# Kernel optimization log

Hardware: AMD Instinct MI355X
Metric: run time of the kernel (lower is better)

The kernel has to match this reference:

```python
import jax, jax.numpy as jnp
import numpy as np

RES = 64
NU = 0.002
DX = 2.0 * np.pi / RES
DT = 0.001
M1 = 12
M2 = 12
WIDTH = 32


def _central(x, axis, dx):
    # periodic central difference via roll (matches torch.roll semantics)
    return (jnp.roll(x, -1, axis) - jnp.roll(x, 1, axis)) / (2.0 * dx)


def _grad_module(u):
    # TurbulenceRCLN.compute_grad_u: central diff in x,y; j==2 branch is u*0.1 (kept faithfully)
    g0 = _central(u, 2, DX)
    g1 = _central(u, 3, DX)
    g2 = u * 0.1
    return jnp.stack([g0, g1, g2], axis=2)  # (B,3,3,N,N,N) indexed [b,i,j]


def _grad_solver(u):
    # NavierStokesSolver._compute_gradient: true central differences in all 3 dirs
    return jnp.stack([_central(u, 2 + j, DX) for j in range(3)], axis=2)


def _laplacian(u):
    lap = jnp.zeros_like(u)
    for ax in (2, 3, 4):
        lap = lap + (jnp.roll(u, -1, ax) - 2.0 * u + jnp.roll(u, 1, ax)) / (DX * DX)
    return lap


def _div_tau(tau):
    # tau: (B,3,3,N,N,N); div_i = sum_j d tau_ij / dx_j
    return sum(_central(tau[:, :, j], 2 + j, DX) for j in range(3))


def _spectral_conv(x, w1, w2):
    # x: (B,C,N,N); w1/w2: (C,C,M1,M2,2) real/imag
    N = x.shape[-1]
    xft = jnp.fft.rfft2(x)  # (B,C,N,N//2+1) complex
    w1c = w1[..., 0] + 1j * w1[..., 1]
    w2c = w2[..., 0] + 1j * w2[..., 1]
    a = jnp.einsum('bixy,ioxy->boxy', xft[:, :, :M1, :M2], w1c)
    b = jnp.einsum('bixy,ioxy->boxy', xft[:, :, -M1:, :M2], w2c)
    out = jnp.zeros_like(xft).at[:, :, :M1, :M2].set(a).at[:, :, -M1:, :M2].set(b)
    return jnp.fft.irfft2(out, s=(N, N))


def _fno2d(x, fc0_w, fc0_b, spec_w1, spec_w2, conv_w, conv_b, fc1_w, fc1_b, fc2_w, fc2_b):
    h = jnp.einsum('bcxy,cd->bdxy', x, fc0_w) + fc0_b[None, :, None, None]
    for l in range(4):
        s = _spectral_conv(h, spec_w1[l], spec_w2[l])
        w = jnp.einsum('bcxy,co->boxy', h, conv_w[l]) + conv_b[l][None, :, None, None]
        h = s + w
        if l < 3:
            h = jax.nn.gelu(h)
    h = jax.nn.gelu(jnp.einsum('bcxy,cd->bdxy', h, fc1_w) + fc1_b[None, :, None, None])
    return jnp.einsum('bcxy,cd->bdxy', h, fc2_w) + fc2_b[None, :, None, None]


def setup_inputs() -> dict:
    key = jax.random.key(0)
    ks = jax.random.split(key, 8)
    B = 16
    scale = 1.0 / (WIDTH * WIDTH)
    return {
        'velocity': jax.random.normal(ks[0], (B, 3, RES, RES, RES), jnp.float32),
        'fc0_w': jax.random.normal(ks[1], (10, WIDTH), jnp.float32) * 0.1,
        'fc0_b': jnp.zeros((WIDTH,), jnp.float32),
        'spec_w1': jax.random.normal(ks[2], (4, WIDTH, WIDTH, M1, M2, 2), jnp.float32) * scale,
        'spec_w2': jax.random.normal(ks[3], (4, WIDTH, WIDTH, M1, M2, 2), jnp.float32) * scale,
        'conv_w': jax.random.normal(ks[4], (4, WIDTH, WIDTH), jnp.float32) * 0.1,
        'conv_b': jnp.zeros((4, WIDTH), jnp.float32),
        'fc1_w': jax.random.normal(ks[5], (WIDTH, 128), jnp.float32) * 0.1,
        'fc1_b': jnp.zeros((128,), jnp.float32),
        'fc2_w': jax.random.normal(ks[6], (128, 6), jnp.float32) * 0.1,
        'fc2_b': jnp.zeros((6,), jnp.float32),
    }


def reference(velocity, fc0_w, fc0_b, spec_w1, spec_w2, conv_w, conv_b, fc1_w, fc1_b, fc2_w, fc2_b):
    B = velocity.shape[0]
    N = RES
    # --- soft-shell closure input ---
    grad_u = _grad_module(velocity)                                   # (B,3,3,N,N,N)
    S = 0.5 * (grad_u + jnp.swapaxes(grad_u, 1, 2))
    S_mag = jnp.sqrt(2.0 * jnp.sum(S * S, axis=(1, 2), keepdims=True))  # (B,1,1,N,N,N)
    g_slice = grad_u[:, :, :, :, N // 2, :].reshape(B, 9, N, N)        # 9 grad channels at mid-plane
    s_slice = S_mag[:, :, :, :, N // 2, :].reshape(B, 1, N, N)         # 1 strain-mag channel
    closure_in = jnp.concatenate([g_slice, s_slice], axis=1)          # (B,10,N,N)
    tau2d = _fno2d(closure_in, fc0_w, fc0_b, spec_w1, spec_w2, conv_w, conv_b,
                   fc1_w, fc1_b, fc2_w, fc2_b)                         # (B,6,N,N)
    t = jnp.broadcast_to(tau2d[..., None], (B, 6, N, N, N))           # expand along z
    # reconstruct symmetric stress tensor (B,3,3,N,N,N)
    row0 = jnp.stack([t[:, 0], t[:, 3], t[:, 4]], axis=1)
    row1 = jnp.stack([t[:, 3], t[:, 1], t[:, 5]], axis=1)
    row2 = jnp.stack([t[:, 4], t[:, 5], t[:, 2]], axis=1)
    tau_full = jnp.stack([row0, row1, row2], axis=1)
    # --- hard-core NS step ---
    g = _grad_solver(velocity)
    lap = _laplacian(velocity)
    convection = jnp.einsum('bixyz,bijxyz->bjxyz', velocity, g)
    div_tau = _div_tau(tau_full)
    return velocity + DT * (-convection + NU * lap + div_tau)
```

## Files before the change

kernel.cpp:

```cpp
#include <hip/hip_runtime.h>
#include <math.h>

#define NRES 64
#define NXY  4096
#define NVOL 262144
#define BB   16
#define WID  32
#define MM   12
#define R24  24

constexpr double DX_d   = 2.0 * 3.14159265358979323846 / 64.0;
constexpr float  INV2DX = (float)(1.0 / (2.0 * DX_d));
constexpr float  INVDX2 = (float)(1.0 / (DX_d * DX_d));
constexpr float  DT_c   = 0.001f;
constexpr float  NU_c   = 0.002f;

constexpr size_t OFF_FR  = 0;
constexpr size_t OFF_FI  = OFF_FR + (size_t)R24 * NRES;
constexpr size_t OFF_GR  = OFF_FI + (size_t)R24 * NRES;
constexpr size_t OFF_GI  = OFF_GR + (size_t)MM * NRES;
constexpr size_t OFF_CL  = OFF_GI + (size_t)MM * NRES;
constexpr size_t OFF_HA  = OFF_CL + (size_t)BB * 10 * NXY;
constexpr size_t OFF_HB  = OFF_HA + (size_t)BB * WID * NXY;
constexpr size_t OFF_T1R = OFF_HB + (size_t)BB * WID * NXY;
constexpr size_t OFF_T1I = OFF_T1R + (size_t)BB * WID * R24 * NRES;
constexpr size_t OFF_XR  = OFF_T1I + (size_t)BB * WID * R24 * NRES;
constexpr size_t OFF_XI  = OFF_XR + (size_t)BB * WID * R24 * MM;
constexpr size_t OFF_MR  = OFF_XI + (size_t)BB * WID * R24 * MM;
constexpr size_t OFF_MI  = OFF_MR + (size_t)BB * WID * R24 * MM;
constexpr size_t OFF_AR  = OFF_MI + (size_t)BB * WID * R24 * MM;
constexpr size_t OFF_AI  = OFF_AR + (size_t)BB * WID * MM * NRES;
constexpr size_t OFF_H1  = OFF_AI + (size_t)BB * WID * MM * NRES;
constexpr size_t OFF_TAU = OFF_H1 + (size_t)BB * 128 * NXY;
constexpr size_t OFF_FRT = OFF_TAU + (size_t)BB * 6 * NXY;
constexpr size_t OFF_FIT = OFF_FRT + (size_t)NRES * R24;

constexpr size_t OFF_SP  = OFF_H1;
constexpr size_t OFF_W1T = OFF_H1 + (size_t)BB * WID * NXY;
constexpr size_t OFF_CWT = OFF_W1T + 4096;
constexpr size_t OFF_W0T = OFF_CWT + 4096;
constexpr size_t OFF_PT  = OFF_T1R;
constexpr size_t PT_STRIDE = (size_t)BB * 6 * NXY;

__device__ __forceinline__ float gelu_fast(float x) {
    float z = 0.79788456080286535588f * (x + 0.044715f * x * x * x);
    float e = __expf(2.0f * z);
    float t = 1.0f - 2.0f / (e + 1.0f);
    return 0.5f * x * (1.0f + t);
}

__global__ void k_setup(const float* __restrict__ fc1w, const float* __restrict__ convw,
                        const float* __restrict__ fc0w, float* __restrict__ ws) {
    int idx = blockIdx.x * 256 + threadIdx.x;
    if (idx < R24 * NRES) {
        int r = idx / NRES, x = idx % NRES;
        int kx = (r < MM) ? r : (r + 40);
        double ang = -2.0 * 3.14159265358979323846 * (double)(kx * x) / 64.0;
        float cr = (float)cos(ang), ci = (float)sin(ang);
        ws[OFF_FR + idx] = cr;
        ws[OFF_FI + idx] = ci;
        ws[OFF_FRT + (size_t)x * R24 + r] = cr;
        ws[OFF_FIT + (size_t)x * R24 + r] = ci;
    }
    if (idx < MM * NRES) {
        int ky = idx / NRES, y = idx % NRES;
        double ang = -2.0 * 3.14159265358979323846 * (double)(ky * y) / 64.0;
        ws[OFF_GR + idx] = (float)cos(ang);
        ws[OFF_GI + idx] = (float)sin(ang);
    }
    if (idx < 4096) {
        int c = idx >> 7, e = idx & 127;
        ws[OFF_W1T + (size_t)e * 32 + c] = fc1w[idx];
    } else if (idx < 8192) {
        int j = idx - 4096;
        int l = j >> 10, r = j & 1023;
        int c = r >> 5, o = r & 31;
        ws[OFF_CWT + (size_t)l * 1024 + o * 32 + c] = convw[j];
    } else if (idx < 8512) {
        int j = idx - 8192;
        int c = j >> 5, d = j & 31;
        ws[OFF_W0T + (size_t)d * 10 + c] = fc0w[j];
    }
}

__global__ void k_closure(const float* __restrict__ v, float* __restrict__ ws) {
    int idx = blockIdx.x * 256 + threadIdx.x;
    int b = idx >> 10;
    int rr = idx & 1023;
    int x = rr >> 4, z0 = (rr & 15) * 4;
    int xp = (x + 1) & 63, xm = (x - 1) & 63;
    float4 g[3][3];
    for (int i = 0; i < 3; i++) {
        const float* vb = v + (((size_t)(b * 3 + i)) << 18);
        float4 u4   = *(const float4*)(vb + (size_t)x  * 4096 + 32 * 64 + z0);
        float4 uxp4 = *(const float4*)(vb + (size_t)xp * 4096 + 32 * 64 + z0);
        float4 uxm4 = *(const float4*)(vb + (size_t)xm * 4096 + 32 * 64 + z0);
        float4 uyp4 = *(const float4*)(vb + (size_t)x  * 4096 + 33 * 64 + z0);
        float4 uym4 = *(const float4*)(vb + (size_t)x  * 4096 + 31 * 64 + z0);
        g[i][0] = make_float4((uxp4.x - uxm4.x) * INV2DX, (uxp4.y - uxm4.y) * INV2DX,
                              (uxp4.z - uxm4.z) * INV2DX, (uxp4.w - uxm4.w) * INV2DX);
        g[i][1] = make_float4((uyp4.x - uym4.x) * INV2DX, (uyp4.y - uym4.y) * INV2DX,
                              (uyp4.z - uym4.z) * INV2DX, (uyp4.w - uym4.w) * INV2DX);
        g[i][2] = make_float4(0.1f * u4.x, 0.1f * u4.y, 0.1f * u4.z, 0.1f * u4.w);
    }
    float4 ss = make_float4(0.f, 0.f, 0.f, 0.f);
    for (int i = 0; i < 3; i++)
        for (int j = 0; j < 3; j++) {
            float4 a = g[i][j], bt = g[j][i];
            float sx = 0.5f * (a.x + bt.x), sy = 0.5f * (a.y + bt.y);
            float sz = 0.5f * (a.z + bt.z), sw_ = 0.5f * (a.w + bt.w);
            ss.x += sx * sx; ss.y += sy * sy; ss.z += sz * sz; ss.w += sw_ * sw_;
        }
    float4 smag = make_float4(sqrtf(2.f * ss.x), sqrtf(2.f * ss.y),
                              sqrtf(2.f * ss.z), sqrtf(2.f * ss.w));
    float* cl = ws + OFF_CL + (size_t)b * 10 * NXY + (size_t)x * 64 + z0;
    for (int i = 0; i < 3; i++)
        for (int j = 0; j < 3; j++)
            *(float4*)(cl + (size_t)(i * 3 + j) * NXY) = g[i][j];
    *(float4*)(cl + (size_t)9 * NXY) = smag;
}

__global__ void k_fc0(const float* __restrict__ cl, const float* __restrict__ w0t,
                      const float* __restrict__ bias, float* __restrict__ h) {
    __shared__ __align__(16) float sw[32 * 12];
    __shared__ float sb[32];
    int tid = threadIdx.x;
    for (int i = tid; i < 320; i += 256) {
        int d = i / 10, c = i % 10;
        sw[d * 12 + c] = w0t[i];
    }
    if (tid < 32) sb[tid] = bias[tid];
    __syncthreads();
    int wid = tid >> 6, lane = tid & 63;
    int q = blockIdx.x * 64 + lane;
    int b = q >> 10, p = (q & 1023) * 4;
    const float* c0 = cl + (size_t)b * 10 * NXY + p;
    float4 cv[10];
#pragma unroll
    for (int c = 0; c < 10; c++) cv[c] = *(const float4*)(c0 + (size_t)c * NXY);
    float* hp = h + (size_t)b * WID * NXY + p;
#pragma unroll
    for (int j = 0; j < 8; j++) {
        int d = wid * 8 + j;
        float4 acc = make_float4(sb[d], sb[d], sb[d], sb[d]);
#pragma unroll
        for (int c = 0; c < 10; c++) {
            float w = sw[d * 12 + c];
            acc.x += w * cv[c].x; acc.y += w * cv[c].y;
            acc.z += w * cv[c].z; acc.w += w * cv[c].w;
        }
        *(float4*)(hp + (size_t)d * NXY) = acc;
    }
}

__global__ void k_fwd(const float* __restrict__ h, const float* __restrict__ ws,
                      float* __restrict__ xr, float* __restrict__ xi) {
    __shared__ __align__(16) float sh[4096];
    __shared__ float st1r[24 * 65];
    __shared__ float st1i[24 * 65];
    int tid = threadIdx.x;
    int bc = blockIdx.x;
    const float4* hp4 = (const float4*)(h + (size_t)bc * NXY);
    float4* sh4 = (float4*)sh;
#pragma unroll
    for (int i = 0; i < 4; i++) sh4[tid + 256 * i] = hp4[tid + 256 * i];
    __syncthreads();
    const float* FRT = ws + OFF_FRT;
    const float* FIT = ws + OFF_FIT;
#pragma unroll
    for (int it = 0; it < 6; it++) {
        int point = it * 256 + tid;
        int y = point & 63;
        int rr = __builtin_amdgcn_readfirstlane(point >> 6);
        float ar = 0.f, ai = 0.f;
#pragma unroll 16
        for (int x = 0; x < 64; x++) {
            float hv = sh[x * 64 + y];
            ar += hv * FRT[x * R24 + rr];
            ai += hv * FIT[x * R24 + rr];
        }
        st1r[rr * 65 + y] = ar;
        st1i[rr * 65 + y] = ai;
    }
    __syncthreads();
    const float* GR = ws + OFF_GR;
    const float* GI = ws + OFF_GI;
#pragma unroll
    for (int it = 0; it < 2; it++) {
        int point = it * 256 + tid;
        if (point < 288) {
            int r = point / 12, ky = point - r * 12;
            const float* Gr = GR + (size_t)ky * 64;
            const float* Gi = GI + (size_t)ky * 64;
            float ar = 0.f, ai = 0.f;
#pragma unroll 16
            for (int y = 0; y < 64; y++) {
                float a = st1r[r * 65 + y], b = st1i[r * 65 + y];
                float c = Gr[y], d = Gi[y];
                ar += a * c - b * d;
                ai += a * d + b * c;
            }
            xr[(size_t)bc * 288 + point] = ar;
            xi[(size_t)bc * 288 + point] = ai;
        }
    }
}

__global__ void k_spec(const float* __restrict__ xr, const float* __restrict__ xi,
                       const float* __restrict__ w1, const float* __restrict__ w2,
                       float* __restrict__ mr, float* __restrict__ mi) {
    int idx = blockIdx.x * 256 + threadIdx.x;
    int ky = idx % 12;
    int t  = idx / 12;
    int r  = t % 24;
    int bo = t / 24;
    int o = bo & 31, b = bo >> 5;
    int kx = (r < 12) ? r : (r - 12);
    const float* wl = (r < 12) ? w1 : w2;
    int kxy = kx * 12 + ky;
    float ar = 0.f, ai = 0.f;
    for (int i = 0; i < 32; i++) {
        size_t xoff = ((size_t)(b * 32 + i) * 24 + r) * 12 + ky;
        float a = xr[xoff], bi_ = xi[xoff];
        const float* wp = wl + ((size_t)(i * 32 + o) * 144 + kxy) * 2;
        float wr_ = wp[0], wi_ = wp[1];
        ar += a * wr_ - bi_ * wi_;
        ai += a * wi_ + bi_ * wr_;
    }
    mr[idx] = ar; mi[idx] = ai;
}

__global__ void k_invf(const float* __restrict__ mr, const float* __restrict__ mi,
                       const float* __restrict__ ws, float* __restrict__ sp) {
    __shared__ float sm_r[288];
    __shared__ float sm_i[288];
    __shared__ float sa_r[12 * 64];
    __shared__ float sa_i[12 * 64];
    int tid = threadIdx.x;
    int bo = blockIdx.x;
    for (int i = tid; i < 288; i += 256) {
        sm_r[i] = mr[(size_t)bo * 288 + i];
        sm_i[i] = mi[(size_t)bo * 288 + i];
    }
    __syncthreads();
    const float* FR = ws + OFF_FR;
    const float* FI = ws + OFF_FI;
#pragma unroll
    for (int it = 0; it < 3; it++) {
        int point = it * 256 + tid;
        int x = point & 63;
        int ky = __builtin_amdgcn_readfirstlane(point >> 6);
        float ar = 0.f, ai = 0.f;
#pragma unroll 8
        for (int r = 0; r < 24; r++) {
            float a = sm_r[r * 12 + ky], b = sm_i[r * 12 + ky];
            float c = FR[r * 64 + x], d = FI[r * 64 + x];
            ar += a * c + b * d;
            ai += b * c - a * d;
        }
        sa_r[ky * 64 + x] = ar;
        sa_i[ky * 64 + x] = ai;
    }
    __syncthreads();
    const float* GR = ws + OFF_GR;
    const float* GI = ws + OFF_GI;
    float* spb = sp + (size_t)bo * NXY;
#pragma unroll
    for (int it = 0; it < 16; it++) {
        int px = it * 256 + tid;
        int y = px & 63;
        int x = __builtin_amdgcn_readfirstlane(px >> 6);
        float s = sa_r[x];
#pragma unroll
        for (int ky = 1; ky < 12; ky++) {
            float gr = GR[ky * 64 + y];
            float gi = GI[ky * 64 + y];
            s += 2.0f * (sa_r[ky * 64 + x] * gr + sa_i[ky * 64 + x] * gi);
        }
        spb[px] = s * (1.0f / 4096.0f);
    }
}

template <int DOGELU>
__global__ void k_convg(const float* __restrict__ sp, const float* __restrict__ hin,
                        const float* __restrict__ cwt, const float* __restrict__ cb,
                        float* __restrict__ hout) {
    __shared__ __align__(16) float scw[1024];
    __shared__ float scb[32];
    int tid = threadIdx.x;
#pragma unroll
    for (int i = 0; i < 4; i++) scw[tid + 256 * i] = cwt[tid + 256 * i];
    if (tid < 32) scb[tid] = cb[tid];
    __syncthreads();
    int wid = tid >> 6, lane = tid & 63;
    int blk = blockIdx.x;
    int osec = blk & 1;
    int pix = (blk >> 1) * 64 + lane;
    int b = pix >> 12, p = pix & 4095;
    const float* hp = hin + (size_t)b * WID * NXY + p;
    float hv[32];
#pragma unroll
    for (int c = 0; c < 32; c++) hv[c] = hp[(size_t)c * NXY];
    const float* spp = sp + (size_t)b * WID * NXY + p;
    float* op = hout + (size_t)b * WID * NXY + p;
#pragma unroll
    for (int j = 0; j < 4; j++) {
        int o = osec * 16 + wid * 4 + j;
        const float4* wr = (const float4*)&scw[o * 32];
        float a0 = 0.f, a1 = 0.f, a2 = 0.f, a3 = 0.f;
#pragma unroll
        for (int q = 0; q < 8; q += 4) {
            float4 w0 = wr[q], w1 = wr[q + 1], w2 = wr[q + 2], w3 = wr[q + 3];
            a0 += w0.x * hv[q * 4]      + w0.y * hv[q * 4 + 1]  + w0.z * hv[q * 4 + 2]  + w0.w * hv[q * 4 + 3];
            a1 += w1.x * hv[q * 4 + 4]  + w1.y * hv[q * 4 + 5]  + w1.z * hv[q * 4 + 6]  + w1.w * hv[q * 4 + 7];
            a2 += w2.x * hv[q * 4 + 8]  + w2.y * hv[q * 4 + 9]  + w2.z * hv[q * 4 + 10] + w2.w * hv[q * 4 + 11];
            a3 += w3.x * hv[q * 4 + 12] + w3.y * hv[q * 4 + 13] + w3.z * hv[q * 4 + 14] + w3.w * hv[q * 4 + 15];
        }
        float v = scb[o] + (a0 + a1) + (a2 + a3) + spp[(size_t)o * NXY];
        if (DOGELU) v = gelu_fast(v);
        op[(size_t)o * NXY] = v;
    }
}

__global__ void k_head(const float* __restrict__ h, const float* __restrict__ w1t,
                       const float* __restrict__ b1, const float* __restrict__ w2,
                       float* __restrict__ pt) {
    __shared__ __align__(16) float sw1[4096];
    __shared__ float sb1[128];
    __shared__ __align__(16) float sw2[128 * 8];
    __shared__ float red[4][6][64];
    int tid = threadIdx.x;
#pragma unroll
    for (int i = 0; i < 16; i++) sw1[tid + 256 * i] = w1t[tid + 256 * i];
    if (tid < 128) sb1[tid] = b1[tid];
    {
        for (int i = tid; i < 768; i += 256) {
            int e = i / 6, t = i - e * 6;
            sw2[e * 8 + t] = w2[i];
        }
    }
    __syncthreads();
    int wid = tid >> 6, lane = tid & 63;
    int blk = blockIdx.x;
    int esec = blk & 1;
    int pix = (blk >> 1) * 64 + lane;
    int b = pix >> 12, p = pix & 4095;
    const float* hp = h + (size_t)b * WID * NXY + p;
    float hv[32];
#pragma unroll
    for (int c = 0; c < 32; c++) hv[c] = hp[(size_t)c * NXY];
    float acc[6] = {0.f, 0.f, 0.f, 0.f, 0.f, 0.f};
#pragma unroll
    for (int jj = 0; jj < 16; jj++) {
        int e = esec * 64 + wid * 16 + jj;
        const float4* wr = (const float4*)&sw1[e * 32];
        float d0 = 0.f, d1 = 0.f, d2 = 0.f, d3 = 0.f;
#pragma unroll
        for (int q = 0; q < 8; q += 4) {
            float4 w0 = wr[q], w1 = wr[q + 1], w2_ = wr[q + 2], w3 = wr[q + 3];
            d0 += w0.x * hv[q * 4]      + w0.y * hv[q * 4 + 1]  + w0.z * hv[q * 4 + 2]  + w0.w * hv[q * 4 + 3];
            d1 += w1.x * hv[q * 4 + 4]  + w1.y * hv[q * 4 + 5]  + w1.z * hv[q * 4 + 6]  + w1.w * hv[q * 4 + 7];
            d2 += w2_.x * hv[q * 4 + 8] + w2_.y * hv[q * 4 + 9] + w2_.z * hv[q * 4 + 10]+ w2_.w * hv[q * 4 + 11];
            d3 += w3.x * hv[q * 4 + 12] + w3.y * hv[q * 4 + 13] + w3.z * hv[q * 4 + 14] + w3.w * hv[q * 4 + 15];
        }
        float d = sb1[e] + (d0 + d1) + (d2 + d3);
        float g = gelu_fast(d);
        const float4* w2r = (const float4*)&sw2[e * 8];
        float4 wa = w2r[0], wb = w2r[1];
        acc[0] += g * wa.x; acc[1] += g * wa.y; acc[2] += g * wa.z;
        acc[3] += g * wa.w; acc[4] += g * wb.x; acc[5] += g * wb.y;
    }
#pragma unroll
    for (int t = 0; t < 6; t++) red[wid][t][lane] = acc[t];
    __syncthreads();
    if (wid == 0) {
        float* pb = pt + (size_t)esec * PT_STRIDE + (size_t)b * 6 * NXY + p;
#pragma unroll
        for (int t = 0; t < 6; t++)
            pb[(size_t)t * NXY] = red[0][t][lane] + red[1][t][lane] +
                                  red[2][t][lane] + red[3][t][lane];
    }
}

__global__ void k_tred(const float* __restrict__ pt, const float* __restrict__ b2,
                       float* __restrict__ tau) {
    int idx = blockIdx.x * 256 + threadIdx.x;
    int t = (idx >> 12) % 6;
    tau[idx] = pt[idx] + pt[idx + PT_STRIDE] + b2[t];
}

__global__ void k_ns(const float* __restrict__ v, const float* __restrict__ tau,
                     float* __restrict__ out) {
    int idx = blockIdx.x * 256 + threadIdx.x;
    int b = idx >> 16;
    int r = idx & 65535;
    int x = r >> 10;
    int y = (r >> 4) & 63;
    int z0 = (r & 15) * 4;
    int xp = (x + 1) & 63, xm = (x - 1) & 63;
    int yp = (y + 1) & 63, ym = (y - 1) & 63;
    int zm = (z0 - 1) & 63, zp = (z0 + 4) & 63;

    float4 u[3], gx[3], gy[3], gz[3], lap[3];
    for (int i = 0; i < 3; i++) {
        const float* vb = v + (((size_t)(b * 3 + i)) << 18);
        const float* row = vb + (size_t)x * 4096 + (size_t)y * 64;
        float4 c4   = *(const float4*)(row + z0);
        float  czm  = row[zm];
        float  czp  = row[zp];
        float4 xp4  = *(const float4*)(vb + (size_t)xp * 4096 + (size_t)y * 64 + z0);
        float4 xm4  = *(const float4*)(vb + (size_t)xm * 4096 + (size_t)y * 64 + z0);
        float4 yp4  = *(const float4*)(vb + (size_t)x * 4096 + (size_t)yp * 64 + z0);
        float4 ym4  = *(const float4*)(vb + (size_t)x * 4096 + (size_t)ym * 64 + z0);
        u[i] = c4;
        gx[i] = make_float4((xp4.x - xm4.x) * INV2DX, (xp4.y - xm4.y) * INV2DX,
                            (xp4.z - xm4.z) * INV2DX, (xp4.w - xm4.w) * INV2DX);
        gy[i] = make_float4((yp4.x - ym4.x) * INV2DX, (yp4.y - ym4.y) * INV2DX,
                            (yp4.z - ym4.z) * INV2DX, (yp4.w - ym4.w) * INV2DX);
        gz[i] = make_float4((c4.y - czm) * INV2DX, (c4.z - c4.x) * INV2DX,
                            (c4.w - c4.y) * INV2DX, (czp - c4.z) * INV2DX);
        lap[i] = make_float4(
            (xp4.x + xm4.x + yp4.x + ym4.x + czm  + c4.y - 6.f * c4.x) * INVDX2,
            (xp4.y + xm4.y + yp4.y + ym4.y + c4.x + c4.z - 6.f * c4.y) * INVDX2,
            (xp4.z + xm4.z + yp4.z + ym4.z + c4.y + c4.w - 6.f * c4.z) * INVDX2,
            (xp4.w + xm4.w + yp4.w + ym4.w + c4.z + czp  - 6.f * c4.w) * INVDX2);
    }
    const float* tb = tau + (size_t)b * 6 * NXY;
    int pxp = xp * 64 + y, pxm = xm * 64 + y, pyp = x * 64 + yp, pym = x * 64 + ym;
    float d0 = (tb[0 * NXY + pxp] - tb[0 * NXY + pxm]) * INV2DX +
               (tb[3 * NXY + pyp] - tb[3 * NXY + pym]) * INV2DX;
    float d1 = (tb[3 * NXY + pxp] - tb[3 * NXY + pxm]) * INV2DX +
               (tb[1 * NXY + pyp] - tb[1 * NXY + pym]) * INV2DX;
    float d2 = (tb[4 * NXY + pxp] - tb[4 * NXY + pxm]) * INV2DX +
               (tb[5 * NXY + pyp] - tb[5 * NXY + pym]) * INV2DX;

    size_t so = ((size_t)b * 3) * NVOL + (size_t)x * 4096 + (size_t)y * 64 + z0;
#pragma unroll
    for (int i = 0; i < 3; i++) {
        float dti = (i == 0) ? d0 : (i == 1) ? d1 : d2;
        float4 conv = make_float4(
            u[0].x * ((i==0)?gx[0].x:(i==1)?gy[0].x:gz[0].x) + u[1].x * ((i==0)?gx[1].x:(i==1)?gy[1].x:gz[1].x) + u[2].x * ((i==0)?gx[2].x:(i==1)?gy[2].x:gz[2].x),
            u[0].y * ((i==0)?gx[0].y:(i==1)?gy[0].y:gz[0].y) + u[1].y * ((i==0)?gx[1].y:(i==1)?gy[1].y:gz[1].y) + u[2].y * ((i==0)?gx[2].y:(i==1)?gy[2].y:gz[2].y),
            u[0].z * ((i==0)?gx[0].z:(i==1)?gy[0].z:gz[0].z) + u[1].z * ((i==0)?gx[1].z:(i==1)?gy[1].z:gz[1].z) + u[2].z * ((i==0)?gx[2].z:(i==1)?gy[2].z:gz[2].z),
            u[0].w * ((i==0)?gx[0].w:(i==1)?gy[0].w:gz[0].w) + u[1].w * ((i==0)?gx[1].w:(i==1)?gy[1].w:gz[1].w) + u[2].w * ((i==0)?gx[2].w:(i==1)?gy[2].w:gz[2].w));
        float4 res = make_float4(
            u[i].x + DT_c * (-conv.x + NU_c * lap[i].x + dti),
            u[i].y + DT_c * (-conv.y + NU_c * lap[i].y + dti),
            u[i].z + DT_c * (-conv.z + NU_c * lap[i].z + dti),
            u[i].w + DT_c * (-conv.w + NU_c * lap[i].w + dti));
        *(float4*)(out + so + (size_t)i * NVOL) = res;
    }
}

extern "C" void kernel_launch(void* const* d_in, const int* in_sizes, int n_in,
                              void* d_out, int out_size, void* d_ws, size_t ws_size,
                              hipStream_t stream) {
    const float* vel   = (const float*)d_in[0];
    const float* fc0w  = (const float*)d_in[1];
    const float* fc0b  = (const float*)d_in[2];
    const float* sw1   = (const float*)d_in[3];
    const float* sw2   = (const float*)d_in[4];
    const float* convw = (const float*)d_in[5];
    const float* convb = (const float*)d_in[6];
    const float* fc1w  = (const float*)d_in[7];
    const float* fc1b  = (const float*)d_in[8];
    const float* fc2w  = (const float*)d_in[9];
    const float* fc2b  = (const float*)d_in[10];
    float* ws  = (float*)d_ws;
    float* out = (float*)d_out;

    k_setup<<<34, 256, 0, stream>>>(fc1w, convw, fc0w, ws);
    k_closure<<<64, 256, 0, stream>>>(vel, ws);
    k_fc0<<<256, 256, 0, stream>>>(ws + OFF_CL, ws + OFF_W0T, fc0b, ws + OFF_HA);

    float* hcur  = ws + OFF_HA;
    float* hnext = ws + OFF_HB;
    for (int l = 0; l < 4; l++) {
        const float* wl1 = sw1 + (size_t)l * WID * WID * MM * MM * 2;
        const float* wl2 = sw2 + (size_t)l * WID * WID * MM * MM * 2;
        const float* cwl = ws + OFF_CWT + (size_t)l * WID * WID;
        const float* cbl = convb + (size_t)l * WID;
        k_fwd<<<512, 256, 0, stream>>>(hcur, ws, ws + OFF_XR, ws + OFF_XI);
        k_spec<<<576, 256, 0, stream>>>(ws + OFF_XR, ws + OFF_XI, wl1, wl2, ws + OFF_MR, ws + OFF_MI);
        k_invf<<<512, 256, 0, stream>>>(ws + OFF_MR, ws + OFF_MI, ws, ws + OFF_SP);
        if (l < 3)
            k_convg<1><<<2048, 256, 0, stream>>>(ws + OFF_SP, hcur, cwl, cbl, hnext);
        else
            k_convg<0><<<2048, 256, 0, stream>>>(ws + OFF_SP, hcur, cwl, cbl, hnext);
        float* tmp = hcur; hcur = hnext; hnext = tmp;
    }

    k_head<<<2048, 256, 0, stream>>>(hcur, ws + OFF_W1T, fc1b, fc2w, ws + OFF_PT);
    k_tred<<<1536, 256, 0, stream>>>(ws + OFF_PT, fc2b, ws + OFF_TAU);
    k_ns<<<4096, 256, 0, stream>>>(vel, ws + OFF_TAU, out);
}
```

Measured before the change: 265.4 us.

## Fuse closure+fc0, spectral mix+inverse FFT, head+reduction; halve conv/head grids

Merges the closure-feature kernel into the fc0 lift, folds the per-mode spectral weight contraction into the inverse-transform kernel, and drops the split-output reduction kernel by having k_head produce all 128 hidden channels and add the bias directly. The conv and head kernels now handle all output channels per block, using half as many blocks. This removes several launches and intermediate global round-trips (closure buffer, mode buffers, partial tau). In exchange the fused kernels run with fewer blocks (closure+fc0 uses only 64 blocks), and the spectral contraction is recomputed per output block, which may lower occupancy and parallelism.

```diff
diff --git a/kernel.cpp b/kernel.cpp
--- a/kernel.cpp
+++ b/kernel.cpp
@@ -39,8 +39,6 @@
 constexpr size_t OFF_W1T = OFF_H1 + (size_t)BB * WID * NXY;
 constexpr size_t OFF_CWT = OFF_W1T + 4096;
 constexpr size_t OFF_W0T = OFF_CWT + 4096;
-constexpr size_t OFF_PT  = OFF_T1R;
-constexpr size_t PT_STRIDE = (size_t)BB * 6 * NXY;
 
 __device__ __forceinline__ float gelu_fast(float x) {
     float z = 0.79788456080286535588f * (x + 0.044715f * x * x * x);
@@ -83,13 +81,23 @@
     }
 }
 
-__global__ void k_closure(const float* __restrict__ v, float* __restrict__ ws) {
-    int idx = blockIdx.x * 256 + threadIdx.x;
+__global__ void k_clfc0(const float* __restrict__ v, const float* __restrict__ w0t,
+                        const float* __restrict__ bias, float* __restrict__ h) {
+    __shared__ __align__(16) float sw[32 * 12];
+    __shared__ float sb[32];
+    int tid = threadIdx.x;
+    for (int i = tid; i < 320; i += 256) {
+        int d = i / 10, c = i % 10;
+        sw[d * 12 + c] = w0t[i];
+    }
+    if (tid < 32) sb[tid] = bias[tid];
+    __syncthreads();
+    int idx = blockIdx.x * 256 + tid;
     int b = idx >> 10;
     int rr = idx & 1023;
     int x = rr >> 4, z0 = (rr & 15) * 4;
     int xp = (x + 1) & 63, xm = (x - 1) & 63;
-    float4 g[3][3];
+    float4 cv[10];
     for (int i = 0; i < 3; i++) {
         const float* vb = v + (((size_t)(b * 3 + i)) << 18);
         float4 u4   = *(const float4*)(vb + (size_t)x  * 4096 + 32 * 64 + z0);
@@ -97,51 +105,25 @@
         float4 uxm4 = *(const float4*)(vb + (size_t)xm * 4096 + 32 * 64 + z0);
         float4 uyp4 = *(const float4*)(vb + (size_t)x  * 4096 + 33 * 64 + z0);
         float4 uym4 = *(const float4*)(vb + (size_t)x  * 4096 + 31 * 64 + z0);
-        g[i][0] = make_float4((uxp4.x - uxm4.x) * INV2DX, (uxp4.y - uxm4.y) * INV2DX,
-                              (uxp4.z - uxm4.z) * INV2DX, (uxp4.w - uxm4.w) * INV2DX);
-        g[i][1] = make_float4((uyp4.x - uym4.x) * INV2DX, (uyp4.y - uym4.y) * INV2DX,
-                              (uyp4.z - uym4.z) * INV2DX, (uyp4.w - uym4.w) * INV2DX);
-        g[i][2] = make_float4(0.1f * u4.x, 0.1f * u4.y, 0.1f * u4.z, 0.1f * u4.w);
+        cv[i * 3 + 0] = make_float4((uxp4.x - uxm4.x) * INV2DX, (uxp4.y - uxm4.y) * INV2DX,
+                                    (uxp4.z - uxm4.z) * INV2DX, (uxp4.w - uxm4.w) * INV2DX);
+        cv[i * 3 + 1] = make_float4((uyp4.x - uym4.x) * INV2DX, (uyp4.y - uym4.y) * INV2DX,
+                                    (uyp4.z - uym4.z) * INV2DX, (uyp4.w - uym4.w) * INV2DX);
+        cv[i * 3 + 2] = make_float4(0.1f * u4.x, 0.1f * u4.y, 0.1f * u4.z, 0.1f * u4.w);
     }
     float4 ss = make_float4(0.f, 0.f, 0.f, 0.f);
     for (int i = 0; i < 3; i++)
         for (int j = 0; j < 3; j++) {
-            float4 a = g[i][j], bt = g[j][i];
+            float4 a = cv[i * 3 + j], bt = cv[j * 3 + i];
             float sx = 0.5f * (a.x + bt.x), sy = 0.5f * (a.y + bt.y);
             float sz = 0.5f * (a.z + bt.z), sw_ = 0.5f * (a.w + bt.w);
             ss.x += sx * sx; ss.y += sy * sy; ss.z += sz * sz; ss.w += sw_ * sw_;
         }
-    float4 smag = make_float4(sqrtf(2.f * ss.x), sqrtf(2.f * ss.y),
-                              sqrtf(2.f * ss.z), sqrtf(2.f * ss.w));
-    float* cl = ws + OFF_CL + (size_t)b * 10 * NXY + (size_t)x * 64 + z0;
-    for (int i = 0; i < 3; i++)
-        for (int j = 0; j < 3; j++)
-            *(float4*)(cl + (size_t)(i * 3 + j) * NXY) = g[i][j];
-    *(float4*)(cl + (size_t)9 * NXY) = smag;
-}
-
-__global__ void k_fc0(const float* __restrict__ cl, const float* __restrict__ w0t,
-                      const float* __restrict__ bias, float* __restrict__ h) {
-    __shared__ __align__(16) float sw[32 * 12];
-    __shared__ float sb[32];
-    int tid = threadIdx.x;
-    for (int i = tid; i < 320; i += 256) {
-        int d = i / 10, c = i % 10;
-        sw[d * 12 + c] = w0t[i];
-    }
-    if (tid < 32) sb[tid] = bias[tid];
-    __syncthreads();
-    int wid = tid >> 6, lane = tid & 63;
-    int q = blockIdx.x * 64 + lane;
-    int b = q >> 10, p = (q & 1023) * 4;
-    const float* c0 = cl + (size_t)b * 10 * NXY + p;
-    float4 cv[10];
-#pragma unroll
-    for (int c = 0; c < 10; c++) cv[c] = *(const float4*)(c0 + (size_t)c * NXY);
-    float* hp = h + (size_t)b * WID * NXY + p;
-#pragma unroll
-    for (int j = 0; j < 8; j++) {
-        int d = wid * 8 + j;
+    cv[9] = make_float4(sqrtf(2.f * ss.x), sqrtf(2.f * ss.y),
+                        sqrtf(2.f * ss.z), sqrtf(2.f * ss.w));
+    float* hp = h + (size_t)b * WID * NXY + (size_t)x * 64 + z0;
+#pragma unroll
+    for (int d = 0; d < 32; d++) {
         float4 acc = make_float4(sb[d], sb[d], sb[d], sb[d]);
 #pragma unroll
         for (int c = 0; c < 10; c++) {
@@ -206,41 +188,32 @@
     }
 }
 
-__global__ void k_spec(const float* __restrict__ xr, const float* __restrict__ xi,
-                       const float* __restrict__ w1, const float* __restrict__ w2,
-                       float* __restrict__ mr, float* __restrict__ mi) {
-    int idx = blockIdx.x * 256 + threadIdx.x;
-    int ky = idx % 12;
-    int t  = idx / 12;
-    int r  = t % 24;
-    int bo = t / 24;
-    int o = bo & 31, b = bo >> 5;
-    int kx = (r < 12) ? r : (r - 12);
-    const float* wl = (r < 12) ? w1 : w2;
-    int kxy = kx * 12 + ky;
-    float ar = 0.f, ai = 0.f;
-    for (int i = 0; i < 32; i++) {
-        size_t xoff = ((size_t)(b * 32 + i) * 24 + r) * 12 + ky;
-        float a = xr[xoff], bi_ = xi[xoff];
-        const float* wp = wl + ((size_t)(i * 32 + o) * 144 + kxy) * 2;
-        float wr_ = wp[0], wi_ = wp[1];
-        ar += a * wr_ - bi_ * wi_;
-        ai += a * wi_ + bi_ * wr_;
-    }
-    mr[idx] = ar; mi[idx] = ai;
-}
-
-__global__ void k_invf(const float* __restrict__ mr, const float* __restrict__ mi,
-                       const float* __restrict__ ws, float* __restrict__ sp) {
+__global__ void k_specinv(const float* __restrict__ xr, const float* __restrict__ xi,
+                          const float* __restrict__ w1, const float* __restrict__ w2,
+                          const float* __restrict__ ws, float* __restrict__ sp) {
     __shared__ float sm_r[288];
     __shared__ float sm_i[288];
     __shared__ float sa_r[12 * 64];
     __shared__ float sa_i[12 * 64];
     int tid = threadIdx.x;
     int bo = blockIdx.x;
-    for (int i = tid; i < 288; i += 256) {
-        sm_r[i] = mr[(size_t)bo * 288 + i];
-        sm_i[i] = mi[(size_t)bo * 288 + i];
+    int o = bo & 31, b = bo >> 5;
+    for (int m = tid; m < 288; m += 256) {
+        int r = m / 12;
+        int kxy = (r < MM) ? m : (m - 144);
+        const float* wp = ((r < MM) ? w1 : w2) + ((size_t)o * 144 + kxy) * 2;
+        size_t xbase = (size_t)b * 32 * 288 + m;
+        float ar = 0.f, ai = 0.f;
+#pragma unroll 8
+        for (int i = 0; i < 32; i++) {
+            float a   = xr[xbase + (size_t)i * 288];
+            float bb  = xi[xbase + (size_t)i * 288];
+            float wr_ = wp[(size_t)i * 9216];
+            float wi_ = wp[(size_t)i * 9216 + 1];
+            ar += a * wr_ - bb * wi_;
+            ai += a * wi_ + bb * wr_;
+        }
+        sm_r[m] = ar; sm_i[m] = ai;
     }
     __syncthreads();
     const float* FR = ws + OFF_FR;
@@ -253,10 +226,10 @@
         float ar = 0.f, ai = 0.f;
 #pragma unroll 8
         for (int r = 0; r < 24; r++) {
-            float a = sm_r[r * 12 + ky], b = sm_i[r * 12 + ky];
+            float a = sm_r[r * 12 + ky], bb = sm_i[r * 12 + ky];
             float c = FR[r * 64 + x], d = FI[r * 64 + x];
-            ar += a * c + b * d;
-            ai += b * c - a * d;
+            ar += a * c + bb * d;
+            ai += bb * c - a * d;
         }
         sa_r[ky * 64 + x] = ar;
         sa_i[ky * 64 + x] = ai;
@@ -293,9 +266,7 @@
     if (tid < 32) scb[tid] = cb[tid];
     __syncthreads();
     int wid = tid >> 6, lane = tid & 63;
-    int blk = blockIdx.x;
-    int osec = blk & 1;
-    int pix = (blk >> 1) * 64 + lane;
+    int pix = blockIdx.x * 64 + lane;
     int b = pix >> 12, p = pix & 4095;
     const float* hp = hin + (size_t)b * WID * NXY + p;
     float hv[32];
@@ -304,8 +275,8 @@
     const float* spp = sp + (size_t)b * WID * NXY + p;
     float* op = hout + (size_t)b * WID * NXY + p;
 #pragma unroll
-    for (int j = 0; j < 4; j++) {
-        int o = osec * 16 + wid * 4 + j;
+    for (int j = 0; j < 8; j++) {
+        int o = wid * 8 + j;
         const float4* wr = (const float4*)&scw[o * 32];
         float a0 = 0.f, a1 = 0.f, a2 = 0.f, a3 = 0.f;
 #pragma unroll
@@ -324,7 +295,7 @@
 
 __global__ void k_head(const float* __restrict__ h, const float* __restrict__ w1t,
                        const float* __restrict__ b1, const float* __restrict__ w2,
-                       float* __restrict__ pt) {
+                       const float* __restrict__ b2, float* __restrict__ tau) {
     __shared__ __align__(16) float sw1[4096];
     __shared__ float sb1[128];
     __shared__ __align__(16) float sw2[128 * 8];
@@ -333,17 +304,13 @@
 #pragma unroll
     for (int i = 0; i < 16; i++) sw1[tid + 256 * i] = w1t[tid + 256 * i];
     if (tid < 128) sb1[tid] = b1[tid];
-    {
-        for (int i = tid; i < 768; i += 256) {
-            int e = i / 6, t = i - e * 6;
-            sw2[e * 8 + t] = w2[i];
-        }
+    for (int i = tid; i < 768; i += 256) {
+        int e = i / 6, t = i - e * 6;
+        sw2[e * 8 + t] = w2[i];
     }
     __syncthreads();
     int wid = tid >> 6, lane = tid & 63;
-    int blk = blockIdx.x;
-    int esec = blk & 1;
-    int pix = (blk >> 1) * 64 + lane;
+    int pix = blockIdx.x * 64 + lane;
     int b = pix >> 12, p = pix & 4095;
     const float* hp = h + (size_t)b * WID * NXY + p;
     float hv[32];
@@ -351,8 +318,8 @@
     for (int c = 0; c < 32; c++) hv[c] = hp[(size_t)c * NXY];
     float acc[6] = {0.f, 0.f, 0.f, 0.f, 0.f, 0.f};
 #pragma unroll
-    for (int jj = 0; jj < 16; jj++) {
-        int e = esec * 64 + wid * 16 + jj;
+    for (int jj = 0; jj < 32; jj++) {
+        int e = wid * 32 + jj;
         const float4* wr = (const float4*)&sw1[e * 32];
         float d0 = 0.f, d1 = 0.f, d2 = 0.f, d3 = 0.f;
 #pragma unroll
@@ -374,19 +341,12 @@
     for (int t = 0; t < 6; t++) red[wid][t][lane] = acc[t];
     __syncthreads();
     if (wid == 0) {
-        float* pb = pt + (size_t)esec * PT_STRIDE + (size_t)b * 6 * NXY + p;
+        float* tb = tau + (size_t)b * 6 * NXY + p;
 #pragma unroll
         for (int t = 0; t < 6; t++)
-            pb[(size_t)t * NXY] = red[0][t][lane] + red[1][t][lane] +
-                                  red[2][t][lane] + red[3][t][lane];
-    }
-}
-
-__global__ void k_tred(const float* __restrict__ pt, const float* __restrict__ b2,
-                       float* __restrict__ tau) {
-    int idx = blockIdx.x * 256 + threadIdx.x;
-    int t = (idx >> 12) % 6;
-    tau[idx] = pt[idx] + pt[idx + PT_STRIDE] + b2[t];
+            tb[(size_t)t * NXY] = red[0][t][lane] + red[1][t][lane] +
+                                  red[2][t][lane] + red[3][t][lane] + b2[t];
+    }
 }
 
 __global__ void k_ns(const float* __restrict__ v, const float* __restrict__ tau,
@@ -470,8 +430,7 @@
     float* out = (float*)d_out;
 
     k_setup<<<34, 256, 0, stream>>>(fc1w, convw, fc0w, ws);
-    k_closure<<<64, 256, 0, stream>>>(vel, ws);
-    k_fc0<<<256, 256, 0, stream>>>(ws + OFF_CL, ws + OFF_W0T, fc0b, ws + OFF_HA);
+    k_clfc0<<<64, 256, 0, stream>>>(vel, ws + OFF_W0T, fc0b, ws + OFF_HA);
 
     float* hcur  = ws + OFF_HA;
     float* hnext = ws + OFF_HB;
@@ -481,16 +440,14 @@
         const float* cwl = ws + OFF_CWT + (size_t)l * WID * WID;
         const float* cbl = convb + (size_t)l * WID;
         k_fwd<<<512, 256, 0, stream>>>(hcur, ws, ws + OFF_XR, ws + OFF_XI);
-        k_spec<<<576, 256, 0, stream>>>(ws + OFF_XR, ws + OFF_XI, wl1, wl2, ws + OFF_MR, ws + OFF_MI);
-        k_invf<<<512, 256, 0, stream>>>(ws + OFF_MR, ws + OFF_MI, ws, ws + OFF_SP);
+        k_specinv<<<512, 256, 0, stream>>>(ws + OFF_XR, ws + OFF_XI, wl1, wl2, ws, ws + OFF_SP);
         if (l < 3)
-            k_convg<1><<<2048, 256, 0, stream>>>(ws + OFF_SP, hcur, cwl, cbl, hnext);
+            k_convg<1><<<1024, 256, 0, stream>>>(ws + OFF_SP, hcur, cwl, cbl, hnext);
         else
-            k_convg<0><<<2048, 256, 0, stream>>>(ws + OFF_SP, hcur, cwl, cbl, hnext);
+            k_convg<0><<<1024, 256, 0, stream>>>(ws + OFF_SP, hcur, cwl, cbl, hnext);
         float* tmp = hcur; hcur = hnext; hnext = tmp;
     }
 
-    k_head<<<2048, 256, 0, stream>>>(hcur, ws + OFF_W1T, fc1b, fc2w, ws + OFF_PT);
-    k_tred<<<1536, 256, 0, stream>>>(ws + OFF_PT, fc2b, ws + OFF_TAU);
+    k_head<<<1024, 256, 0, stream>>>(hcur, ws + OFF_W1T, fc1b, fc2w, fc2b, ws + OFF_TAU);
     k_ns<<<4096, 256, 0, stream>>>(vel, ws + OFF_TAU, out);
 }
```

New measurement: 249.2 us. 6.1% less time.
